# Kernel optimization log

Hardware: AMD Instinct MI355X
Metric: run time of the kernel (lower is better)

## Reference

```python
import jax, jax.numpy as jnp
import numpy as np


def setup_inputs() -> dict:
    key = jax.random.key(0)
    ingredients = jax.random.normal(key, (16, 1024, 1024), dtype=jnp.float32)
    return {"ingredients": ingredients}


def reference(ingredients) -> jnp.ndarray:
    # ingredients: [B, H, W]
    # Output [B, H, W, 5]: channel 0 = center, 1 = up (j-1), 2 = right (k+1),
    # 3 = down (j+1), 4 = left (k-1). At grid borders the original falls back
    # to the CENTER value (padding = ingredients[i][j][k]), which is exactly
    # edge-replication of the center pixel into the missing neighbor slot.
    x = ingredients
    center = x
    up = jnp.concatenate([x[:, :1, :], x[:, :-1, :]], axis=1)    # row 0 -> its own center
    down = jnp.concatenate([x[:, 1:, :], x[:, -1:, :]], axis=1)  # last row -> its own center
    left = jnp.concatenate([x[:, :, :1], x[:, :, :-1]], axis=2)  # col 0 -> its own center
    right = jnp.concatenate([x[:, :, 1:], x[:, :, -1:]], axis=2) # last col -> its own center
    return jnp.stack([center, up, right, down, left], axis=-1)
```

## Files before the change

### kernel.cpp

```cpp
#include <hip/hip_runtime.h>


typedef float f4 __attribute__((ext_vector_type(4)));

__global__ __launch_bounds__(256) void stencil5_kernel(
    const float* __restrict__ in, float* __restrict__ out) {
    constexpr int W = 1024;
    constexpr int H = 1024;

    __shared__ float lds[256 * 20];

    const int i   = threadIdx.x;
    const int row = blockIdx.x;
    const int k0  = i << 2;
    const int j   = row & (H - 1);

    const long base = ((long)row << 10);
    const float* prow = in + base + k0;

    const float4 c = *(const float4*)prow;

    const float* uptr = prow - ((j > 0)     ? W : 0);
    const float* dptr = prow + ((j < H - 1) ? W : 0);
    const float4 u = *(const float4*)uptr;
    const float4 d = *(const float4*)dptr;

    float lx = prow[-(k0 > 0 ? 1 : 0)];
    lx = (k0 > 0) ? lx : c.x;
    float rw = prow[(k0 + 4 < W) ? 4 : 3];
    rw = (k0 + 4 < W) ? rw : c.w;

    float4* l = (float4*)(lds + i * 20);
    l[0] = make_float4(c.x, u.x, c.y, d.x);
    l[1] = make_float4(lx,  c.y, u.y, c.z);
    l[2] = make_float4(d.y, c.x, c.z, u.z);
    l[3] = make_float4(c.w, d.z, c.y, c.w);
    l[4] = make_float4(u.w, rw,  d.w, c.z);

    __syncthreads();

    const f4* ls = (const f4*)lds;
    f4* o = (f4*)(out + base * 5);
    #pragma unroll
    for (int r = 0; r < 5; ++r) {
        __builtin_nontemporal_store(ls[i + 256 * r], o + i + 256 * r);
    }
}

extern "C" void kernel_launch(void* const* d_in, const int* in_sizes, int n_in,
                              void* d_out, int out_size, void* d_ws, size_t ws_size,
                              hipStream_t stream) {
    const float* in = (const float*)d_in[0];
    float* out = (float*)d_out;

    const int n = in_sizes[0];
    const int blocks = n >> 10;

    stencil5_kernel<<<blocks, 256, 0, stream>>>(in, out);
}
```

Measured before the change: 367.5 us.

## Process eight rows per block with rolling up/center/down register window

Each block now handles eight consecutive rows and keeps the up, current and down row vectors in registers, rotating them so each input row is loaded once per block instead of three times. A next-row prefetch is issued each iteration. In exchange, the grid has eight times fewer blocks, and each row iteration adds an extra barrier so the shared staging buffer can be reused.

After: 378.7 us. 1.03x slower.

```diff
diff --git a/kernel.cpp b/kernel.cpp
--- a/kernel.cpp
+++ b/kernel.cpp
@@ -2,6 +2,8 @@
 
 
 typedef float f4 __attribute__((ext_vector_type(4)));
+
+constexpr int ROWS = 8;
 
 __global__ __launch_bounds__(256) void stencil5_kernel(
     const float* __restrict__ in, float* __restrict__ out) {
@@ -10,40 +12,52 @@
 
     __shared__ float lds[256 * 20];
 
-    const int i   = threadIdx.x;
-    const int row = blockIdx.x;
-    const int k0  = i << 2;
-    const int j   = row & (H - 1);
+    const int i  = threadIdx.x;
+    const int k0 = i << 2;
+    const int g0 = blockIdx.x * ROWS;
+    const int j0 = g0 & (H - 1);
+    const long imgbase = (long)(g0 - j0) << 10;
 
-    const long base = ((long)row << 10);
-    const float* prow = in + base + k0;
+    const float* pk = in + imgbase + k0;
 
-    const float4 c = *(const float4*)prow;
+    float4 up  = *(const float4*)(pk + ((long)(j0 > 0 ? j0 - 1 : 0) << 10));
+    float4 cur = *(const float4*)(pk + ((long)j0 << 10));
+    float4 dwn = *(const float4*)(pk + ((long)(j0 + 1) << 10));
 
-    const float* uptr = prow - ((j > 0)     ? W : 0);
-    const float* dptr = prow + ((j < H - 1) ? W : 0);
-    const float4 u = *(const float4*)uptr;
-    const float4 d = *(const float4*)dptr;
+    f4* o = (f4*)(out + ((long)g0 << 10) * 5);
+    float4* l = (float4*)(lds + i * 20);
+    const f4* ls = (const f4*)lds;
 
-    float lx = prow[-(k0 > 0 ? 1 : 0)];
-    lx = (k0 > 0) ? lx : c.x;
-    float rw = prow[(k0 + 4 < W) ? 4 : 3];
-    rw = (k0 + 4 < W) ? rw : c.w;
+    #pragma unroll
+    for (int r = 0; r < ROWS; ++r) {
+        const int j = j0 + r;
 
-    float4* l = (float4*)(lds + i * 20);
-    l[0] = make_float4(c.x, u.x, c.y, d.x);
-    l[1] = make_float4(lx,  c.y, u.y, c.z);
-    l[2] = make_float4(d.y, c.x, c.z, u.z);
-    l[3] = make_float4(c.w, d.z, c.y, c.w);
-    l[4] = make_float4(u.w, rw,  d.w, c.z);
+        const int jn = (j + 2 < H) ? (j + 2) : (H - 1);
+        const float4 nxt = *(const float4*)(pk + ((long)jn << 10));
 
-    __syncthreads();
+        const float* pc = pk + ((long)j << 10);
+        float lx = pc[k0 > 0 ? -1 : 0];
+        lx = (k0 > 0) ? lx : cur.x;
+        float rw = pc[(k0 + 4 < W) ? 4 : 3];
+        rw = (k0 + 4 < W) ? rw : cur.w;
 
-    const f4* ls = (const f4*)lds;
-    f4* o = (f4*)(out + base * 5);
-    #pragma unroll
-    for (int r = 0; r < 5; ++r) {
-        __builtin_nontemporal_store(ls[i + 256 * r], o + i + 256 * r);
+        l[0] = make_float4(cur.x, up.x,  cur.y, dwn.x);
+        l[1] = make_float4(lx,    cur.y, up.y,  cur.z);
+        l[2] = make_float4(dwn.y, cur.x, cur.z, up.z);
+        l[3] = make_float4(cur.w, dwn.z, cur.y, cur.w);
+        l[4] = make_float4(up.w,  rw,    dwn.w, cur.z);
+
+        __syncthreads();
+
+        #pragma unroll
+        for (int s = 0; s < 5; ++s) {
+            __builtin_nontemporal_store(ls[i + 256 * s],
+                                        o + (long)r * 1280 + i + 256 * s);
+        }
+
+        __syncthreads();
+
+        up = cur; cur = dwn; dwn = nxt;
     }
 }
 
@@ -54,7 +68,8 @@
     float* out = (float*)d_out;
 
     const int n = in_sizes[0];
-    const int blocks = n >> 10;
+    const int rows = n >> 10;
+    const int blocks = rows / ROWS;
 
     stencil5_kernel<<<blocks, 256, 0, stream>>>(in, out);
 }
```
